# Kernel tuning notes

Measured on AMD Instinct MI355X. Metric: run time of the kernel, lower is better.

The kernel has to match this reference:

```python
import jax, jax.numpy as jnp
import numpy as np

N_NODES = 100000
BN_EPS = 1e-5


def gcn_conv(x, W, b, row, col, n_nodes):
    """GCNConv: D^{-1/2}(A+I)D^{-1/2} X W + b, edges row->col."""
    h = x @ W  # [N, out]
    # degree with self-loops, counted on destination side (symmetric for undirected)
    deg = jax.ops.segment_sum(jnp.ones(row.shape[0], dtype=x.dtype), col,
                              num_segments=n_nodes) + 1.0
    dis = jax.lax.rsqrt(deg)  # deg^{-1/2}
    coef = dis[row] * dis[col]  # [E]
    msg = h[row] * coef[:, None]  # gather + scale, [E, out]
    agg = jax.ops.segment_sum(msg, col, num_segments=n_nodes)
    # self-loop contribution: norm = dis[i]*dis[i]
    out = agg + h * (dis * dis)[:, None] + b
    return out


def batchnorm_train(x, gamma, beta):
    mean = jnp.mean(x, axis=0)
    var = jnp.mean(jnp.square(x - mean), axis=0)  # biased, training mode
    return (x - mean) * jax.lax.rsqrt(var + BN_EPS) * gamma + beta


def setup_inputs() -> dict:
    key = jax.random.key(0)
    ks = jax.random.split(key, 8)
    latent_dim, hidden_dim, input_dim = 64, 128, 128
    n_edges = 1600000
    x = jax.random.normal(ks[0], (N_NODES, latent_dim), dtype=jnp.float32)
    edge_index = jax.random.randint(ks[1], (2, n_edges), 0, N_NODES, dtype=jnp.int64)
    s1 = 1.0 / np.sqrt(latent_dim)
    s2 = 1.0 / np.sqrt(hidden_dim)
    W1 = jax.random.uniform(ks[2], (latent_dim, hidden_dim), jnp.float32, -s1, s1)
    b1 = jax.random.uniform(ks[3], (hidden_dim,), jnp.float32, -s1, s1)
    gamma = jnp.ones((hidden_dim,), jnp.float32)
    beta = jnp.zeros((hidden_dim,), jnp.float32)
    W2 = jax.random.uniform(ks[4], (hidden_dim, input_dim), jnp.float32, -s2, s2)
    b2 = jax.random.uniform(ks[5], (input_dim,), jnp.float32, -s2, s2)
    return {"quantized_f_embedding": x, "edge_index": edge_index,
            "W1": W1, "b1": b1, "gamma": gamma, "beta": beta,
            "W2": W2, "b2": b2}


def reference(quantized_f_embedding, edge_index, W1, b1, gamma, beta, W2, b2):
    row, col = edge_index[0], edge_index[1]
    h = gcn_conv(quantized_f_embedding, W1, b1, row, col, N_NODES)
    h = batchnorm_train(h, gamma, beta)
    out = gcn_conv(h, W2, b2, row, col, N_NODES)
    return out
```

## Files before the change

### kernel.cpp

```cpp
#include <hip/hip_runtime.h>

#define NN 100000
#define BN_EPS 1e-5f
#define NBK 782
#define CAP 2560
#define TILE 4096

#define NREP 16
#define CVT_BLKS 6250
#define AGG_BLKS 6250
#define ZERO_BLKS 80
#define PACK1_BLKS 32

typedef __attribute__((ext_vector_type(4))) _Float16 half4;
typedef __attribute__((ext_vector_type(8))) _Float16 half8;
typedef __attribute__((ext_vector_type(4))) float f32x4;


__global__ __launch_bounds__(256) void k_prep0(int* __restrict__ bcur,
                                               float* __restrict__ stats,
                                               const float* __restrict__ W1,
                                               _Float16* __restrict__ wp1) {
    const int b = blockIdx.x;
    const int t = threadIdx.x;
    if (b < ZERO_BLKS) {
        int i = b * 256 + t;
        if (i < 16384) bcur[i] = 0;
        else stats[i - 16384] = 0.f;
    } else {
        int i = (b - ZERO_BLKS) * 256 + t;
        int j = i & 7, l = (i >> 3) & 63, nt = (i >> 9) & 7, kt = i >> 12;
        int k = kt * 32 + ((l >> 4) << 3) + j;
        int n = nt * 16 + (l & 15);
        wp1[i] = (_Float16)W1[k * 128 + n];
    }
}


__global__ __launch_bounds__(256) void k_binc(const int* __restrict__ row,
                                              const int* __restrict__ col,
                                              int* __restrict__ bcur,
                                              int* __restrict__ ebuf,
                                              int E, int binBlks,
                                              const float* __restrict__ x,
                                              _Float16* __restrict__ xh) {
    __shared__ int hist[1024];
    __shared__ int excl[1024];
    __shared__ int cur[1024];
    __shared__ int gbase[1024];
    __shared__ int sc[256];
    __shared__ int staged[TILE];
    __shared__ unsigned short bkt[TILE];
    const int t = threadIdx.x;

    if (blockIdx.x >= binBlks) {
        int i = (blockIdx.x - binBlks) * 256 + t;
        float4 v = reinterpret_cast<const float4*>(x)[i];
        half4 o;
        o.x = (_Float16)v.x; o.y = (_Float16)v.y;
        o.z = (_Float16)v.z; o.w = (_Float16)v.w;
        reinterpret_cast<half4*>(xh)[i] = o;
        return;
    }

    const int base = blockIdx.x * TILE;
    const int nE = min(TILE, E - base);

    #pragma unroll
    for (int q = 0; q < 4; ++q) { hist[q * 256 + t] = 0; cur[q * 256 + t] = 0; }
    __syncthreads();

    int er[16], ec[16];
    #pragma unroll
    for (int k = 0; k < 16; ++k) {
        int idx = base + k * 256 + t;
        if (idx < E) {
            er[k] = row[idx];
            ec[k] = col[idx];
            atomicAdd(&hist[ec[k] >> 7], 1);
        } else {
            ec[k] = -1;
        }
    }
    __syncthreads();

    int h0 = hist[4 * t], h1 = hist[4 * t + 1], h2 = hist[4 * t + 2], h3 = hist[4 * t + 3];
    int p = h0 + h1 + h2 + h3;
    sc[t] = p;
    __syncthreads();
    for (int off = 1; off < 256; off <<= 1) {
        int add = (t >= off) ? sc[t - off] : 0;
        __syncthreads();
        sc[t] += add;
        __syncthreads();
    }
    int e0 = sc[t] - p;
    excl[4 * t]     = e0;
    excl[4 * t + 1] = e0 + h0;
    excl[4 * t + 2] = e0 + h0 + h1;
    excl[4 * t + 3] = e0 + h0 + h1 + h2;
    __syncthreads();

    for (int b = t; b < NBK; b += 256) {
        int h = hist[b];
        gbase[b] = h ? atomicAdd(&bcur[b * 16], h) : 0;
    }

    #pragma unroll
    for (int k = 0; k < 16; ++k) {
        int c = ec[k];
        if (c < 0) continue;
        int b = c >> 7;
        int slot = excl[b] + atomicAdd(&cur[b], 1);
        staged[slot] = (er[k] << 7) | (c & 127);
        bkt[slot] = (unsigned short)b;
    }
    __syncthreads();

    for (int i = t; i < nE; i += 256) {
        int b = bkt[i];
        int off = gbase[b] + (i - excl[b]);
        if (off < CAP) ebuf[b * CAP + off] = staged[i];
    }
}


__global__ __launch_bounds__(256) void k_csr(const int* __restrict__ bcur,
                                             const int* __restrict__ ebuf,
                                             int* __restrict__ rows,
                                             int* __restrict__ start,
                                             int* __restrict__ cnt,
                                             float* __restrict__ dis) {
    __shared__ int hist[128];
    __shared__ int lstart[128];
    __shared__ int cur[128];
    __shared__ int sc[256];
    const int b = blockIdx.x;
    const int t = threadIdx.x;
    const int fill = min(bcur[b * 16], CAP);

    if (t < 128) { hist[t] = 0; cur[t] = 0; }
    __syncthreads();

    int er[CAP / 256];
    #pragma unroll
    for (int k = 0; k < CAP / 256; ++k) {
        int i = k * 256 + t;
        if (i < fill) {
            er[k] = ebuf[b * CAP + i];
            atomicAdd(&hist[er[k] & 127], 1);
        }
    }
    __syncthreads();

    int v = (t < 128) ? hist[t] : 0;
    sc[t] = v;
    __syncthreads();
    for (int off = 1; off < 256; off <<= 1) {
        int add = (t >= off) ? sc[t - off] : 0;
        __syncthreads();
        sc[t] += add;
        __syncthreads();
    }
    if (t < 128) {
        lstart[t] = sc[t] - v;
        const int node = b * 128 + t;
        if (node < NN) {
            start[node] = b * CAP + (sc[t] - v);
            cnt[node] = v;
            dis[node] = rsqrtf((float)(v + 1));
        }
    }
    __syncthreads();

    #pragma unroll
    for (int k = 0; k < CAP / 256; ++k) {
        int i = k * 256 + t;
        if (i < fill) {
            int lc = er[k] & 127;
            int lpos = atomicAdd(&cur[lc], 1);
            rows[b * CAP + lstart[lc] + lpos] = er[k] >> 7;
        }
    }
}


__device__ __forceinline__ void fma_h4(float4& a, half4 v, float c) {
    a.x = fmaf((float)v.x, c, a.x);
    a.y = fmaf((float)v.y, c, a.y);
    a.z = fmaf((float)v.z, c, a.z);
    a.w = fmaf((float)v.w, c, a.w);
}

template<bool SUMC>
__device__ __forceinline__ void agg_body(int blk,
                                         const _Float16* __restrict__ xh,
                                         const int* __restrict__ rows,
                                         const int* __restrict__ start,
                                         const int* __restrict__ cnt,
                                         const float* __restrict__ dis,
                                         _Float16* __restrict__ agg,
                                         float* __restrict__ sumcoef) {
    constexpr int L = 16;
    const int t = threadIdx.x;
    const int g = t / L;
    const int fid = t % L;
    const int n = blk * 16 + g;
    if (n >= NN) return;
    const int s = start[n];
    const int c = cnt[n];
    const float dn = dis[n];
    const half4* X4 = reinterpret_cast<const half4*>(xh);
    half4 hv = X4[n * L + fid];
    const float dn2 = dn * dn;
    float4 acc = make_float4(dn2 * (float)hv.x, dn2 * (float)hv.y,
                             dn2 * (float)hv.z, dn2 * (float)hv.w);
    float sd = 0.f;
    const int* rp = rows + s;
    int k = 0;
    for (; k + 4 <= c; k += 4) {
        int r0 = rp[k], r1 = rp[k + 1], r2 = rp[k + 2], r3 = rp[k + 3];
        float d0 = dis[r0], d1 = dis[r1], d2 = dis[r2], d3 = dis[r3];
        half4 v0 = X4[r0 * L + fid];
        half4 v1 = X4[r1 * L + fid];
        half4 v2 = X4[r2 * L + fid];
        half4 v3 = X4[r3 * L + fid];
        fma_h4(acc, v0, d0 * dn);
        fma_h4(acc, v1, d1 * dn);
        fma_h4(acc, v2, d2 * dn);
        fma_h4(acc, v3, d3 * dn);
        sd += (d0 + d1) + (d2 + d3);
    }
    for (; k < c; ++k) {
        int r = rp[k];
        float dr = dis[r];
        half4 v = X4[r * L + fid];
        fma_h4(acc, v, dr * dn);
        sd += dr;
    }
    half4 o;
    o.x = (_Float16)acc.x; o.y = (_Float16)acc.y;
    o.z = (_Float16)acc.z; o.w = (_Float16)acc.w;
    reinterpret_cast<half4*>(agg)[n * L + fid] = o;
    if (SUMC && fid == 0) sumcoef[n] = dn * sd + dn2;
}


__device__ __forceinline__ void l2prep_body(int bb,
                                            const float* __restrict__ stats,
                                            const float* __restrict__ gamma,
                                            const float* __restrict__ beta,
                                            const float* __restrict__ b1,
                                            const float* __restrict__ W1,
                                            const float* __restrict__ W2,
                                            _Float16* __restrict__ wp12,
                                            float* __restrict__ sv) {
    __shared__ float s_[128];
    __shared__ float f2_[128];
    const int t = threadIdx.x;
    if (t < 128) {
        float sum = 0.f, sum2 = 0.f;
        #pragma unroll
        for (int r = 0; r < NREP; ++r) {
            sum  += stats[r * 256 + t];
            sum2 += stats[r * 256 + 128 + t];
        }
        const float n = (float)NN;
        float mean = sum / n;
        float var = sum2 / n - mean * mean;
        float sc = gamma[t] * rsqrtf(var + BN_EPS);
        s_[t] = sc;
        f2_[t] = b1[t] * sc + (beta[t] - mean * sc);
    }
    __syncthreads();
    if (bb < 32) {
        int i = bb * 256 + t;
        int j = i & 7, l = (i >> 3) & 63, nt = (i >> 9) & 7, kt = i >> 12;
        int kk = kt * 32 + ((l >> 4) << 3) + j;
        int nn = nt * 16 + (l & 15);
        float acc = 0.f;
        #pragma unroll 8
        for (int m = 0; m < 128; ++m)
            acc = fmaf(W1[kk * 128 + m] * s_[m], W2[m * 128 + nn], acc);
        wp12[i] = (_Float16)acc;
    } else if (t < 128) {
        float acc = 0.f;
        for (int k = 0; k < 128; ++k) acc = fmaf(f2_[k], W2[k * 128 + t], acc);
        sv[t] = acc;
    }
}


__global__ __launch_bounds__(256) void k_aggy(const _Float16* __restrict__ xh,
                                              const int* __restrict__ rows,
                                              const int* __restrict__ start,
                                              const int* __restrict__ cnt,
                                              const float* __restrict__ dis,
                                              _Float16* __restrict__ agg,
                                              float* __restrict__ sumcoef) {
    agg_body<true>(blockIdx.x, xh, rows, start, cnt, dis, agg, sumcoef);
}


__global__ __launch_bounds__(256) void k_aggz(const _Float16* __restrict__ y,
                                              const int* __restrict__ rows,
                                              const int* __restrict__ start,
                                              const int* __restrict__ cnt,
                                              const float* __restrict__ dis,
                                              _Float16* __restrict__ z,
                                              const float* __restrict__ stats,
                                              const float* __restrict__ gamma,
                                              const float* __restrict__ beta,
                                              const float* __restrict__ b1,
                                              const float* __restrict__ W1,
                                              const float* __restrict__ W2,
                                              _Float16* __restrict__ wp12,
                                              float* __restrict__ sv) {
    if (blockIdx.x < AGG_BLKS) {
        agg_body<false>(blockIdx.x, y, rows, start, cnt, dis, z, nullptr);
    } else {
        l2prep_body(blockIdx.x - AGG_BLKS, stats, gamma, beta, b1, W1, W2,
                    wp12, sv);
    }
}


template<bool FINAL>
__global__ __launch_bounds__(256) void k_mgemm(const _Float16* __restrict__ A,
                                               const _Float16* __restrict__ Wp,
                                               const float* __restrict__ bias,
                                               const float* __restrict__ sv,
                                               const float* __restrict__ sumcoef,
                                               float* __restrict__ out32,
                                               float* __restrict__ stats) {
    const int t = threadIdx.x;
    const int wv = t >> 6;
    const int ln = t & 63;
    const int cgrp = ln >> 4;
    const int ncol = ln & 15;
    const int r0 = blockIdx.x * 64 + wv * 16;
    const int arow = min(r0 + ncol, NN - 1);

    f32x4 acc[8];
    #pragma unroll
    for (int nt = 0; nt < 8; ++nt) acc[nt] = {0.f, 0.f, 0.f, 0.f};

    const half8* Ap = reinterpret_cast<const half8*>(A + arow * 64 + cgrp * 8);
    const half8* Bp = reinterpret_cast<const half8*>(Wp);

    #pragma unroll
    for (int kt = 0; kt < 2; ++kt) {
        half8 a = Ap[kt * 4];
        #pragma unroll
        for (int nt = 0; nt < 8; ++nt) {
            half8 b = Bp[(kt * 8 + nt) * 64 + ln];
            acc[nt] = __builtin_amdgcn_mfma_f32_16x16x32_f16(a, b, acc[nt], 0, 0, 0);
        }
    }

    if constexpr (!FINAL) {
        __shared__ float ls[4][128];
        __shared__ float ls2[4][128];
        #pragma unroll
        for (int nt = 0; nt < 8; ++nt) {
            const int n = nt * 16 + ncol;
            const float bn = bias[n];
            float s = 0.f, s2 = 0.f;
            #pragma unroll
            for (int j = 0; j < 4; ++j) {
                int gr = r0 + cgrp * 4 + j;
                float v = acc[nt][j] + bn;
                if (gr < NN) {
                    s += v;
                    s2 += v * v;
                }
            }
            s  += __shfl_xor(s, 16);  s  += __shfl_xor(s, 32);
            s2 += __shfl_xor(s2, 16); s2 += __shfl_xor(s2, 32);
            if (ln < 16) { ls[wv][n] = s; ls2[wv][n] = s2; }
        }
        __syncthreads();
        float* rep = stats + (blockIdx.x & (NREP - 1)) * 256;
        if (t < 128) {
            atomicAdd(&rep[t], ls[0][t] + ls[1][t] + ls[2][t] + ls[3][t]);
        } else {
            int u = t - 128;
            atomicAdd(&rep[128 + u], ls2[0][u] + ls2[1][u] + ls2[2][u] + ls2[3][u]);
        }
    } else {
        __shared__ float st[4][16][132];
        float scj[4];
        #pragma unroll
        for (int j = 0; j < 4; ++j) scj[j] = sumcoef[min(r0 + cgrp * 4 + j, NN - 1)];
        #pragma unroll
        for (int nt = 0; nt < 8; ++nt) {
            const int n = nt * 16 + ncol;
            const float svn = sv[n];
            const float bn = bias[n];
            #pragma unroll
            for (int j = 0; j < 4; ++j)
                st[wv][cgrp * 4 + j][n] = acc[nt][j] + scj[j] * svn + bn;
        }
        __syncthreads();
        #pragma unroll
        for (int i = 0; i < 8; ++i) {
            int idx = i * 64 + ln;
            int rr = idx >> 5;
            int c4 = idx & 31;
            int gr = r0 + rr;
            if (gr < NN) {
                float4 v = *reinterpret_cast<float4*>(&st[wv][rr][c4 * 4]);
                *reinterpret_cast<float4*>(&out32[gr * 128 + c4 * 4]) = v;
            }
        }
    }
}


extern "C" void kernel_launch(void* const* d_in, const int* in_sizes, int n_in,
                              void* d_out, int out_size, void* d_ws, size_t ws_size,
                              hipStream_t stream) {
    const float* x     = (const float*)d_in[0];
    const int*   ei    = (const int*)d_in[1];
    const float* W1    = (const float*)d_in[2];
    const float* b1    = (const float*)d_in[3];
    const float* gamma = (const float*)d_in[4];
    const float* beta  = (const float*)d_in[5];
    const float* W2    = (const float*)d_in[6];
    const float* b2    = (const float*)d_in[7];
    float* out = (float*)d_out;

    const int E = in_sizes[1] / 2;
    const int* row = ei;
    const int* col = ei + E;
    const int binBlks = (E + TILE - 1) / TILE;

    int*   bcur    = (int*)d_ws;
    int*   cnt     = bcur + 16384;
    int*   start   = cnt + 102400;
    float* dis     = (float*)(start + 102400);
    float* stats   = dis + 102400;
    float* sv      = stats + 4096;
    float* sumcoef = stats + 5120;
    _Float16* wp1  = (_Float16*)(sumcoef + 102400);
    _Float16* wp12 = wp1 + 8192;
    int*   rows    = (int*)(wp12 + 8192);
    int*   Rbase   = rows + NBK * CAP;
    _Float16* xh   = (_Float16*)Rbase;
    int*   ebuf    = Rbase + 3276800;
    _Float16* y    = (_Float16*)(ebuf + NBK * CAP);
    _Float16* z    = xh;

    k_prep0<<<ZERO_BLKS + PACK1_BLKS, 256, 0, stream>>>(bcur, stats, W1, wp1);
    k_binc<<<binBlks + CVT_BLKS, 256, 0, stream>>>(row, col, bcur, ebuf, E,
                                                   binBlks, x, xh);
    k_csr<<<NBK, 256, 0, stream>>>(bcur, ebuf, rows, start, cnt, dis);

    k_aggy<<<AGG_BLKS, 256, 0, stream>>>(xh, rows, start, cnt, dis, y, sumcoef);
    k_mgemm<false><<<(NN + 63) / 64, 256, 0, stream>>>(y, wp1, b1, nullptr,
                                                       nullptr, nullptr, stats);

    k_aggz<<<AGG_BLKS + 33, 256, 0, stream>>>(y, rows, start, cnt, dis, z,
                                              stats, gamma, beta, b1, W1, W2,
                                              wp12, sv);

    k_mgemm<true><<<(NN + 63) / 64, 256, 0, stream>>>(z, wp12, b2, sv,
                                                      sumcoef, out, nullptr);
}
```

Measured before the change: 147.6 us.

## Fuse neighbor aggregation into MFMA GEMM kernels via shared-memory tile

```diff
diff --git a/kernel.cpp b/kernel.cpp
--- a/kernel.cpp
+++ b/kernel.cpp
@@ -8,33 +8,12 @@
 
 #define NREP 16
 #define CVT_BLKS 6250
-#define AGG_BLKS 6250
-#define ZERO_BLKS 80
 #define PACK1_BLKS 32
+#define GEMM_BLKS 1563
 
 typedef __attribute__((ext_vector_type(4))) _Float16 half4;
 typedef __attribute__((ext_vector_type(8))) _Float16 half8;
 typedef __attribute__((ext_vector_type(4))) float f32x4;
-
-
-__global__ __launch_bounds__(256) void k_prep0(int* __restrict__ bcur,
-                                               float* __restrict__ stats,
-                                               const float* __restrict__ W1,
-                                               _Float16* __restrict__ wp1) {
-    const int b = blockIdx.x;
-    const int t = threadIdx.x;
-    if (b < ZERO_BLKS) {
-        int i = b * 256 + t;
-        if (i < 16384) bcur[i] = 0;
-        else stats[i - 16384] = 0.f;
-    } else {
-        int i = (b - ZERO_BLKS) * 256 + t;
-        int j = i & 7, l = (i >> 3) & 63, nt = (i >> 9) & 7, kt = i >> 12;
-        int k = kt * 32 + ((l >> 4) << 3) + j;
-        int n = nt * 16 + (l & 15);
-        wp1[i] = (_Float16)W1[k * 128 + n];
-    }
-}
 
 
 __global__ __launch_bounds__(256) void k_binc(const int* __restrict__ row,
@@ -43,7 +22,9 @@
                                               int* __restrict__ ebuf,
                                               int E, int binBlks,
                                               const float* __restrict__ x,
-                                              _Float16* __restrict__ xh) {
+                                              _Float16* __restrict__ xh,
+                                              const float* __restrict__ W1,
+                                              _Float16* __restrict__ wp1) {
     __shared__ int hist[1024];
     __shared__ int excl[1024];
     __shared__ int cur[1024];
@@ -54,12 +35,21 @@
     const int t = threadIdx.x;
 
     if (blockIdx.x >= binBlks) {
-        int i = (blockIdx.x - binBlks) * 256 + t;
-        float4 v = reinterpret_cast<const float4*>(x)[i];
-        half4 o;
-        o.x = (_Float16)v.x; o.y = (_Float16)v.y;
-        o.z = (_Float16)v.z; o.w = (_Float16)v.w;
-        reinterpret_cast<half4*>(xh)[i] = o;
+        int rb = blockIdx.x - binBlks;
+        if (rb < CVT_BLKS) {
+            int i = rb * 256 + t;
+            float4 v = reinterpret_cast<const float4*>(x)[i];
+            half4 o;
+            o.x = (_Float16)v.x; o.y = (_Float16)v.y;
+            o.z = (_Float16)v.z; o.w = (_Float16)v.w;
+            reinterpret_cast<half4*>(xh)[i] = o;
+        } else {
+            int i = (rb - CVT_BLKS) * 256 + t;
+            int j = i & 7, l = (i >> 3) & 63, nt = (i >> 9) & 7, kt = i >> 12;
+            int k = kt * 32 + ((l >> 4) << 3) + j;
+            int n = nt * 16 + (l & 15);
+            wp1[i] = (_Float16)W1[k * 128 + n];
+        }
         return;
     }
 
@@ -185,78 +175,17 @@
 }
 
 
-__device__ __forceinline__ void fma_h4(float4& a, half4 v, float c) {
-    a.x = fmaf((float)v.x, c, a.x);
-    a.y = fmaf((float)v.y, c, a.y);
-    a.z = fmaf((float)v.z, c, a.z);
-    a.w = fmaf((float)v.w, c, a.w);
-}
-
-template<bool SUMC>
-__device__ __forceinline__ void agg_body(int blk,
-                                         const _Float16* __restrict__ xh,
-                                         const int* __restrict__ rows,
-                                         const int* __restrict__ start,
-                                         const int* __restrict__ cnt,
-                                         const float* __restrict__ dis,
-                                         _Float16* __restrict__ agg,
-                                         float* __restrict__ sumcoef) {
-    constexpr int L = 16;
-    const int t = threadIdx.x;
-    const int g = t / L;
-    const int fid = t % L;
-    const int n = blk * 16 + g;
-    if (n >= NN) return;
-    const int s = start[n];
-    const int c = cnt[n];
-    const float dn = dis[n];
-    const half4* X4 = reinterpret_cast<const half4*>(xh);
-    half4 hv = X4[n * L + fid];
-    const float dn2 = dn * dn;
-    float4 acc = make_float4(dn2 * (float)hv.x, dn2 * (float)hv.y,
-                             dn2 * (float)hv.z, dn2 * (float)hv.w);
-    float sd = 0.f;
-    const int* rp = rows + s;
-    int k = 0;
-    for (; k + 4 <= c; k += 4) {
-        int r0 = rp[k], r1 = rp[k + 1], r2 = rp[k + 2], r3 = rp[k + 3];
-        float d0 = dis[r0], d1 = dis[r1], d2 = dis[r2], d3 = dis[r3];
-        half4 v0 = X4[r0 * L + fid];
-        half4 v1 = X4[r1 * L + fid];
-        half4 v2 = X4[r2 * L + fid];
-        half4 v3 = X4[r3 * L + fid];
-        fma_h4(acc, v0, d0 * dn);
-        fma_h4(acc, v1, d1 * dn);
-        fma_h4(acc, v2, d2 * dn);
-        fma_h4(acc, v3, d3 * dn);
-        sd += (d0 + d1) + (d2 + d3);
-    }
-    for (; k < c; ++k) {
-        int r = rp[k];
-        float dr = dis[r];
-        half4 v = X4[r * L + fid];
-        fma_h4(acc, v, dr * dn);
-        sd += dr;
-    }
-    half4 o;
-    o.x = (_Float16)acc.x; o.y = (_Float16)acc.y;
-    o.z = (_Float16)acc.z; o.w = (_Float16)acc.w;
-    reinterpret_cast<half4*>(agg)[n * L + fid] = o;
-    if (SUMC && fid == 0) sumcoef[n] = dn * sd + dn2;
-}
-
-
-__device__ __forceinline__ void l2prep_body(int bb,
-                                            const float* __restrict__ stats,
-                                            const float* __restrict__ gamma,
-                                            const float* __restrict__ beta,
-                                            const float* __restrict__ b1,
-                                            const float* __restrict__ W1,
-                                            const float* __restrict__ W2,
-                                            _Float16* __restrict__ wp12,
-                                            float* __restrict__ sv) {
+__global__ __launch_bounds__(256) void k_l2prep(const float* __restrict__ stats,
+                                                const float* __restrict__ gamma,
+                                                const float* __restrict__ beta,
+                                                const float* __restrict__ b1,
+                                                const float* __restrict__ W1,
+                                                const float* __restrict__ W2,
+                                                _Float16* __restrict__ wp12,
+                                                float* __restrict__ sv) {
     __shared__ float s_[128];
     __shared__ float f2_[128];
+    const int bb = blockIdx.x;
     const int t = threadIdx.x;
     if (t < 128) {
         float sum = 0.f, sum2 = 0.f;
@@ -291,66 +220,101 @@
 }
 
 
-__global__ __launch_bounds__(256) void k_aggy(const _Float16* __restrict__ xh,
-                                              const int* __restrict__ rows,
-                                              const int* __restrict__ start,
-                                              const int* __restrict__ cnt,
-                                              const float* __restrict__ dis,
-                                              _Float16* __restrict__ agg,
-                                              float* __restrict__ sumcoef) {
-    agg_body<true>(blockIdx.x, xh, rows, start, cnt, dis, agg, sumcoef);
-}
-
-
-__global__ __launch_bounds__(256) void k_aggz(const _Float16* __restrict__ y,
-                                              const int* __restrict__ rows,
-                                              const int* __restrict__ start,
-                                              const int* __restrict__ cnt,
-                                              const float* __restrict__ dis,
-                                              _Float16* __restrict__ z,
-                                              const float* __restrict__ stats,
-                                              const float* __restrict__ gamma,
-                                              const float* __restrict__ beta,
-                                              const float* __restrict__ b1,
-                                              const float* __restrict__ W1,
-                                              const float* __restrict__ W2,
-                                              _Float16* __restrict__ wp12,
-                                              float* __restrict__ sv) {
-    if (blockIdx.x < AGG_BLKS) {
-        agg_body<false>(blockIdx.x, y, rows, start, cnt, dis, z, nullptr);
-    } else {
-        l2prep_body(blockIdx.x - AGG_BLKS, stats, gamma, beta, b1, W1, W2,
-                    wp12, sv);
-    }
-}
-
+__device__ __forceinline__ void fma_h4(float4& a, half4 v, float c) {
+    a.x = fmaf((float)v.x, c, a.x);
+    a.y = fmaf((float)v.y, c, a.y);
+    a.z = fmaf((float)v.z, c, a.z);
+    a.w = fmaf((float)v.w, c, a.w);
+}
 
 template<bool FINAL>
-__global__ __launch_bounds__(256) void k_mgemm(const _Float16* __restrict__ A,
+__global__ __launch_bounds__(256) void k_agemm(const _Float16* __restrict__ X,
+                                               const int* __restrict__ rows,
+                                               const int* __restrict__ start,
+                                               const int* __restrict__ cnt,
+                                               const float* __restrict__ dis,
                                                const _Float16* __restrict__ Wp,
                                                const float* __restrict__ bias,
                                                const float* __restrict__ sv,
-                                               const float* __restrict__ sumcoef,
+                                               const float* __restrict__ sumcoef_in,
+                                               _Float16* __restrict__ yout,
+                                               float* __restrict__ sumcoef_out,
                                                float* __restrict__ out32,
                                                float* __restrict__ stats) {
+    __shared__ __align__(16) _Float16 tile[64][72];
     const int t = threadIdx.x;
+    const int r0 = blockIdx.x * 64;
+
+    {
+        const int g = t >> 4;
+        const int fid = t & 15;
+        const half4* X4 = reinterpret_cast<const half4*>(X);
+        #pragma unroll
+        for (int q = 0; q < 4; ++q) {
+            const int n = r0 + q * 16 + g;
+            const int lr = q * 16 + g;
+            if (n < NN) {
+                const int s = start[n];
+                const int c = cnt[n];
+                const float dn = dis[n];
+                half4 hv = X4[n * 16 + fid];
+                const float dn2 = dn * dn;
+                float4 acc = make_float4(dn2 * (float)hv.x, dn2 * (float)hv.y,
+                                         dn2 * (float)hv.z, dn2 * (float)hv.w);
+                float sd = 0.f;
+                const int* rp = rows + s;
+                int k = 0;
+                for (; k + 4 <= c; k += 4) {
+                    int rr0 = rp[k], rr1 = rp[k + 1], rr2 = rp[k + 2], rr3 = rp[k + 3];
+                    float d0 = dis[rr0], d1 = dis[rr1], d2 = dis[rr2], d3 = dis[rr3];
+                    half4 v0 = X4[rr0 * 16 + fid];
+                    half4 v1 = X4[rr1 * 16 + fid];
+                    half4 v2 = X4[rr2 * 16 + fid];
+                    half4 v3 = X4[rr3 * 16 + fid];
+                    fma_h4(acc, v0, d0 * dn);
+                    fma_h4(acc, v1, d1 * dn);
+                    fma_h4(acc, v2, d2 * dn);
+                    fma_h4(acc, v3, d3 * dn);
+                    sd += (d0 + d1) + (d2 + d3);
+                }
+                for (; k < c; ++k) {
+                    int r = rp[k];
+                    float dr = dis[r];
+                    half4 v = X4[r * 16 + fid];
+                    fma_h4(acc, v, dr * dn);
+                    sd += dr;
+                }
+                half4 o;
+                o.x = (_Float16)acc.x; o.y = (_Float16)acc.y;
+                o.z = (_Float16)acc.z; o.w = (_Float16)acc.w;
+                *reinterpret_cast<half4*>(&tile[lr][fid * 4]) = o;
+                if constexpr (!FINAL) {
+                    reinterpret_cast<half4*>(yout)[n * 16 + fid] = o;
+                    if (fid == 0) sumcoef_out[n] = dn * sd + dn2;
+                }
+            } else {
+                half4 zz = {(_Float16)0.f, (_Float16)0.f, (_Float16)0.f, (_Float16)0.f};
+                *reinterpret_cast<half4*>(&tile[lr][fid * 4]) = zz;
+            }
+        }
+    }
+    __syncthreads();
+
     const int wv = t >> 6;
     const int ln = t & 63;
     const int cgrp = ln >> 4;
     const int ncol = ln & 15;
-    const int r0 = blockIdx.x * 64 + wv * 16;
-    const int arow = min(r0 + ncol, NN - 1);
+    const int row0 = r0 + wv * 16;
 
     f32x4 acc[8];
     #pragma unroll
     for (int nt = 0; nt < 8; ++nt) acc[nt] = {0.f, 0.f, 0.f, 0.f};
 
-    const half8* Ap = reinterpret_cast<const half8*>(A + arow * 64 + cgrp * 8);
     const half8* Bp = reinterpret_cast<const half8*>(Wp);
 
     #pragma unroll
     for (int kt = 0; kt < 2; ++kt) {
-        half8 a = Ap[kt * 4];
+        half8 a = *reinterpret_cast<const half8*>(&tile[wv * 16 + ncol][kt * 32 + cgrp * 8]);
         #pragma unroll
         for (int nt = 0; nt < 8; ++nt) {
             half8 b = Bp[(kt * 8 + nt) * 64 + ln];
@@ -368,7 +332,7 @@
             float s = 0.f, s2 = 0.f;
             #pragma unroll
             for (int j = 0; j < 4; ++j) {
-                int gr = r0 + cgrp * 4 + j;
+                int gr = row0 + cgrp * 4 + j;
                 float v = acc[nt][j] + bn;
                 if (gr < NN) {
                     s += v;
@@ -388,29 +352,18 @@
             atomicAdd(&rep[128 + u], ls2[0][u] + ls2[1][u] + ls2[2][u] + ls2[3][u]);
         }
     } else {
-        __shared__ float st[4][16][132];
         float scj[4];
         #pragma unroll
-        for (int j = 0; j < 4; ++j) scj[j] = sumcoef[min(r0 + cgrp * 4 + j, NN - 1)];
+        for (int j = 0; j < 4; ++j) scj[j] = sumcoef_in[min(row0 + cgrp * 4 + j, NN - 1)];
         #pragma unroll
         for (int nt = 0; nt < 8; ++nt) {
             const int n = nt * 16 + ncol;
             const float svn = sv[n];
             const float bn = bias[n];
             #pragma unroll
-            for (int j = 0; j < 4; ++j)
-                st[wv][cgrp * 4 + j][n] = acc[nt][j] + scj[j] * svn + bn;
-        }
-        __syncthreads();
-        #pragma unroll
-        for (int i = 0; i < 8; ++i) {
-            int idx = i * 64 + ln;
-            int rr = idx >> 5;
-            int c4 = idx & 31;
-            int gr = r0 + rr;
-            if (gr < NN) {
-                float4 v = *reinterpret_cast<float4*>(&st[wv][rr][c4 * 4]);
-                *reinterpret_cast<float4*>(&out32[gr * 128 + c4 * 4]) = v;
+            for (int j = 0; j < 4; ++j) {
+                int gr = row0 + cgrp * 4 + j;
+                if (gr < NN) out32[gr * 128 + n] = acc[nt][j] + scj[j] * svn + bn;
             }
         }
     }
@@ -436,12 +389,12 @@
     const int binBlks = (E + TILE - 1) / TILE;
 
     int*   bcur    = (int*)d_ws;
-    int*   cnt     = bcur + 16384;
+    float* stats   = (float*)(bcur + 16384);
+    int*   cnt     = (int*)(stats + 4096);
     int*   start   = cnt + 102400;
     float* dis     = (float*)(start + 102400);
-    float* stats   = dis + 102400;
-    float* sv      = stats + 4096;
-    float* sumcoef = stats + 5120;
+    float* sv      = dis + 102400;
+    float* sumcoef = sv + 1024;
     _Float16* wp1  = (_Float16*)(sumcoef + 102400);
     _Float16* wp12 = wp1 + 8192;
     int*   rows    = (int*)(wp12 + 8192);
@@ -449,21 +402,19 @@
     _Float16* xh   = (_Float16*)Rbase;
     int*   ebuf    = Rbase + 3276800;
     _Float16* y    = (_Float16*)(ebuf + NBK * CAP);
-    _Float16* z    = xh;
-
-    k_prep0<<<ZERO_BLKS + PACK1_BLKS, 256, 0, stream>>>(bcur, stats, W1, wp1);
-    k_binc<<<binBlks + CVT_BLKS, 256, 0, stream>>>(row, col, bcur, ebuf, E,
-                                                   binBlks, x, xh);
+
+    hipMemsetAsync(bcur, 0, 20480 * sizeof(int), stream);
+    k_binc<<<binBlks + CVT_BLKS + PACK1_BLKS, 256, 0, stream>>>(
+        row, col, bcur, ebuf, E, binBlks, x, xh, W1, wp1);
     k_csr<<<NBK, 256, 0, stream>>>(bcur, ebuf, rows, start, cnt, dis);
 
-    k_aggy<<<AGG_BLKS, 256, 0, stream>>>(xh, rows, start, cnt, dis, y, sumcoef);
-    k_mgemm<false><<<(NN + 63) / 64, 256, 0, stream>>>(y, wp1, b1, nullptr,
-                                                       nullptr, nullptr, stats);
-
-    k_aggz<<<AGG_BLKS + 33, 256, 0, stream>>>(y, rows, start, cnt, dis, z,
-                                              stats, gamma, beta, b1, W1, W2,
-                                              wp12, sv);
-
-    k_mgemm<true><<<(NN + 63) / 64, 256, 0, stream>>>(z, wp12, b2, sv,
-                                                      sumcoef, out, nullptr);
-}
+    k_agemm<false><<<GEMM_BLKS, 256, 0, stream>>>(xh, rows, start, cnt, dis,
+                                                  wp1, b1, nullptr, nullptr,
+                                                  y, sumcoef, nullptr, stats);
+
+    k_l2prep<<<33, 256, 0, stream>>>(stats, gamma, beta, b1, W1, W2, wp12, sv);
+
+    k_agemm<true><<<GEMM_BLKS, 256, 0, stream>>>(y, rows, start, cnt, dis,
+                                                 wp12, b2, sv, sumcoef,
+                                                 nullptr, nullptr, out, nullptr);
+}
```

Measured after the change: 190.4 us. +29.0%, slower.

## Fuse BN-stats GEMM with second aggregation using a device-wide completion counter

Applied to the files above, without the earlier changes.

```diff
diff --git a/kernel.cpp b/kernel.cpp
--- a/kernel.cpp
+++ b/kernel.cpp
@@ -9,32 +9,15 @@
 #define NREP 16
 #define CVT_BLKS 6250
 #define AGG_BLKS 6250
-#define ZERO_BLKS 80
 #define PACK1_BLKS 32
+#define STATS_BLKS 1563
+
+#define COMBO_L2_OFF (STATS_BLKS + AGG_BLKS)
+#define COMBO_BLKS (COMBO_L2_OFF + 33)
 
 typedef __attribute__((ext_vector_type(4))) _Float16 half4;
 typedef __attribute__((ext_vector_type(8))) _Float16 half8;
 typedef __attribute__((ext_vector_type(4))) float f32x4;
-
-
-__global__ __launch_bounds__(256) void k_prep0(int* __restrict__ bcur,
-                                               float* __restrict__ stats,
-                                               const float* __restrict__ W1,
-                                               _Float16* __restrict__ wp1) {
-    const int b = blockIdx.x;
-    const int t = threadIdx.x;
-    if (b < ZERO_BLKS) {
-        int i = b * 256 + t;
-        if (i < 16384) bcur[i] = 0;
-        else stats[i - 16384] = 0.f;
-    } else {
-        int i = (b - ZERO_BLKS) * 256 + t;
-        int j = i & 7, l = (i >> 3) & 63, nt = (i >> 9) & 7, kt = i >> 12;
-        int k = kt * 32 + ((l >> 4) << 3) + j;
-        int n = nt * 16 + (l & 15);
-        wp1[i] = (_Float16)W1[k * 128 + n];
-    }
-}
 
 
 __global__ __launch_bounds__(256) void k_binc(const int* __restrict__ row,
@@ -43,7 +26,9 @@
                                               int* __restrict__ ebuf,
                                               int E, int binBlks,
                                               const float* __restrict__ x,
-                                              _Float16* __restrict__ xh) {
+                                              _Float16* __restrict__ xh,
+                                              const float* __restrict__ W1,
+                                              _Float16* __restrict__ wp1) {
     __shared__ int hist[1024];
     __shared__ int excl[1024];
     __shared__ int cur[1024];
@@ -54,12 +39,21 @@
     const int t = threadIdx.x;
 
     if (blockIdx.x >= binBlks) {
-        int i = (blockIdx.x - binBlks) * 256 + t;
-        float4 v = reinterpret_cast<const float4*>(x)[i];
-        half4 o;
-        o.x = (_Float16)v.x; o.y = (_Float16)v.y;
-        o.z = (_Float16)v.z; o.w = (_Float16)v.w;
-        reinterpret_cast<half4*>(xh)[i] = o;
+        int rb = blockIdx.x - binBlks;
+        if (rb < CVT_BLKS) {
+            int i = rb * 256 + t;
+            float4 v = reinterpret_cast<const float4*>(x)[i];
+            half4 o;
+            o.x = (_Float16)v.x; o.y = (_Float16)v.y;
+            o.z = (_Float16)v.z; o.w = (_Float16)v.w;
+            reinterpret_cast<half4*>(xh)[i] = o;
+        } else {
+            int i = (rb - CVT_BLKS) * 256 + t;
+            int j = i & 7, l = (i >> 3) & 63, nt = (i >> 9) & 7, kt = i >> 12;
+            int k = kt * 32 + ((l >> 4) << 3) + j;
+            int n = nt * 16 + (l & 15);
+            wp1[i] = (_Float16)W1[k * 128 + n];
+        }
         return;
     }
 
@@ -246,51 +240,6 @@
 }
 
 
-__device__ __forceinline__ void l2prep_body(int bb,
-                                            const float* __restrict__ stats,
-                                            const float* __restrict__ gamma,
-                                            const float* __restrict__ beta,
-                                            const float* __restrict__ b1,
-                                            const float* __restrict__ W1,
-                                            const float* __restrict__ W2,
-                                            _Float16* __restrict__ wp12,
-                                            float* __restrict__ sv) {
-    __shared__ float s_[128];
-    __shared__ float f2_[128];
-    const int t = threadIdx.x;
-    if (t < 128) {
-        float sum = 0.f, sum2 = 0.f;
-        #pragma unroll
-        for (int r = 0; r < NREP; ++r) {
-            sum  += stats[r * 256 + t];
-            sum2 += stats[r * 256 + 128 + t];
-        }
-        const float n = (float)NN;
-        float mean = sum / n;
-        float var = sum2 / n - mean * mean;
-        float sc = gamma[t] * rsqrtf(var + BN_EPS);
-        s_[t] = sc;
-        f2_[t] = b1[t] * sc + (beta[t] - mean * sc);
-    }
-    __syncthreads();
-    if (bb < 32) {
-        int i = bb * 256 + t;
-        int j = i & 7, l = (i >> 3) & 63, nt = (i >> 9) & 7, kt = i >> 12;
-        int kk = kt * 32 + ((l >> 4) << 3) + j;
-        int nn = nt * 16 + (l & 15);
-        float acc = 0.f;
-        #pragma unroll 8
-        for (int m = 0; m < 128; ++m)
-            acc = fmaf(W1[kk * 128 + m] * s_[m], W2[m * 128 + nn], acc);
-        wp12[i] = (_Float16)acc;
-    } else if (t < 128) {
-        float acc = 0.f;
-        for (int k = 0; k < 128; ++k) acc = fmaf(f2_[k], W2[k * 128 + t], acc);
-        sv[t] = acc;
-    }
-}
-
-
 __global__ __launch_bounds__(256) void k_aggy(const _Float16* __restrict__ xh,
                                               const int* __restrict__ rows,
                                               const int* __restrict__ start,
@@ -302,69 +251,56 @@
 }
 
 
-__global__ __launch_bounds__(256) void k_aggz(const _Float16* __restrict__ y,
-                                              const int* __restrict__ rows,
-                                              const int* __restrict__ start,
-                                              const int* __restrict__ cnt,
-                                              const float* __restrict__ dis,
-                                              _Float16* __restrict__ z,
-                                              const float* __restrict__ stats,
-                                              const float* __restrict__ gamma,
-                                              const float* __restrict__ beta,
-                                              const float* __restrict__ b1,
-                                              const float* __restrict__ W1,
-                                              const float* __restrict__ W2,
-                                              _Float16* __restrict__ wp12,
-                                              float* __restrict__ sv) {
-    if (blockIdx.x < AGG_BLKS) {
-        agg_body<false>(blockIdx.x, y, rows, start, cnt, dis, z, nullptr);
-    } else {
-        l2prep_body(blockIdx.x - AGG_BLKS, stats, gamma, beta, b1, W1, W2,
-                    wp12, sv);
-    }
-}
-
-
-template<bool FINAL>
-__global__ __launch_bounds__(256) void k_mgemm(const _Float16* __restrict__ A,
-                                               const _Float16* __restrict__ Wp,
-                                               const float* __restrict__ bias,
-                                               const float* __restrict__ sv,
-                                               const float* __restrict__ sumcoef,
-                                               float* __restrict__ out32,
-                                               float* __restrict__ stats) {
+__global__ __launch_bounds__(256) void k_combo(const _Float16* __restrict__ y,
+                                               const int* __restrict__ rows,
+                                               const int* __restrict__ start,
+                                               const int* __restrict__ cnt,
+                                               const float* __restrict__ dis,
+                                               _Float16* __restrict__ z,
+                                               const _Float16* __restrict__ wp1,
+                                               const float* __restrict__ b1,
+                                               float* __restrict__ stats,
+                                               int* __restrict__ done,
+                                               const float* __restrict__ gamma,
+                                               const float* __restrict__ beta,
+                                               const float* __restrict__ W1,
+                                               const float* __restrict__ W2,
+                                               _Float16* __restrict__ wp12,
+                                               float* __restrict__ sv) {
+    const int bid = blockIdx.x;
     const int t = threadIdx.x;
-    const int wv = t >> 6;
-    const int ln = t & 63;
-    const int cgrp = ln >> 4;
-    const int ncol = ln & 15;
-    const int r0 = blockIdx.x * 64 + wv * 16;
-    const int arow = min(r0 + ncol, NN - 1);
-
-    f32x4 acc[8];
-    #pragma unroll
-    for (int nt = 0; nt < 8; ++nt) acc[nt] = {0.f, 0.f, 0.f, 0.f};
-
-    const half8* Ap = reinterpret_cast<const half8*>(A + arow * 64 + cgrp * 8);
-    const half8* Bp = reinterpret_cast<const half8*>(Wp);
-
-    #pragma unroll
-    for (int kt = 0; kt < 2; ++kt) {
-        half8 a = Ap[kt * 4];
+
+    if (bid < STATS_BLKS) {
+        const int wv = t >> 6;
+        const int ln = t & 63;
+        const int cgrp = ln >> 4;
+        const int ncol = ln & 15;
+        const int r0 = bid * 64 + wv * 16;
+        const int arow = min(r0 + ncol, NN - 1);
+
+        f32x4 acc[8];
         #pragma unroll
-        for (int nt = 0; nt < 8; ++nt) {
-            half8 b = Bp[(kt * 8 + nt) * 64 + ln];
-            acc[nt] = __builtin_amdgcn_mfma_f32_16x16x32_f16(a, b, acc[nt], 0, 0, 0);
-        }
-    }
-
-    if constexpr (!FINAL) {
+        for (int nt = 0; nt < 8; ++nt) acc[nt] = {0.f, 0.f, 0.f, 0.f};
+
+        const half8* Ap = reinterpret_cast<const half8*>(y + arow * 64 + cgrp * 8);
+        const half8* Bp = reinterpret_cast<const half8*>(wp1);
+
+        #pragma unroll
+        for (int kt = 0; kt < 2; ++kt) {
+            half8 a = Ap[kt * 4];
+            #pragma unroll
+            for (int nt = 0; nt < 8; ++nt) {
+                half8 b = Bp[(kt * 8 + nt) * 64 + ln];
+                acc[nt] = __builtin_amdgcn_mfma_f32_16x16x32_f16(a, b, acc[nt], 0, 0, 0);
+            }
+        }
+
         __shared__ float ls[4][128];
         __shared__ float ls2[4][128];
         #pragma unroll
         for (int nt = 0; nt < 8; ++nt) {
             const int n = nt * 16 + ncol;
-            const float bn = bias[n];
+            const float bn = b1[n];
             float s = 0.f, s2 = 0.f;
             #pragma unroll
             for (int j = 0; j < 4; ++j) {
@@ -380,38 +316,119 @@
             if (ln < 16) { ls[wv][n] = s; ls2[wv][n] = s2; }
         }
         __syncthreads();
-        float* rep = stats + (blockIdx.x & (NREP - 1)) * 256;
+        float* rep = stats + (bid & (NREP - 1)) * 256;
         if (t < 128) {
             atomicAdd(&rep[t], ls[0][t] + ls[1][t] + ls[2][t] + ls[3][t]);
         } else {
             int u = t - 128;
             atomicAdd(&rep[128 + u], ls2[0][u] + ls2[1][u] + ls2[2][u] + ls2[3][u]);
         }
+        __syncthreads();
+        __threadfence();
+        if (t == 0) atomicAdd(done, 1);
+    } else if (bid < COMBO_L2_OFF) {
+        agg_body<false>(bid - STATS_BLKS, y, rows, start, cnt, dis, z, nullptr);
     } else {
-        __shared__ float st[4][16][132];
-        float scj[4];
-        #pragma unroll
-        for (int j = 0; j < 4; ++j) scj[j] = sumcoef[min(r0 + cgrp * 4 + j, NN - 1)];
+        const int bb = bid - COMBO_L2_OFF;
+        if (t == 0) {
+            while (__hip_atomic_load(done, __ATOMIC_ACQUIRE,
+                                     __HIP_MEMORY_SCOPE_AGENT) < STATS_BLKS)
+                __builtin_amdgcn_s_sleep(10);
+        }
+        __syncthreads();
+
+        __shared__ float s_[128];
+        __shared__ float f2_[128];
+        if (t < 128) {
+            float sum = 0.f, sum2 = 0.f;
+            #pragma unroll
+            for (int r = 0; r < NREP; ++r) {
+                sum  += __hip_atomic_load(&stats[r * 256 + t], __ATOMIC_RELAXED,
+                                          __HIP_MEMORY_SCOPE_AGENT);
+                sum2 += __hip_atomic_load(&stats[r * 256 + 128 + t], __ATOMIC_RELAXED,
+                                          __HIP_MEMORY_SCOPE_AGENT);
+            }
+            const float n = (float)NN;
+            float mean = sum / n;
+            float var = sum2 / n - mean * mean;
+            float sc = gamma[t] * rsqrtf(var + BN_EPS);
+            s_[t] = sc;
+            f2_[t] = b1[t] * sc + (beta[t] - mean * sc);
+        }
+        __syncthreads();
+        if (bb < 32) {
+            int i = bb * 256 + t;
+            int j = i & 7, l = (i >> 3) & 63, nt = (i >> 9) & 7, kt = i >> 12;
+            int kk = kt * 32 + ((l >> 4) << 3) + j;
+            int nn = nt * 16 + (l & 15);
+            float acc = 0.f;
+            #pragma unroll 8
+            for (int m = 0; m < 128; ++m)
+                acc = fmaf(W1[kk * 128 + m] * s_[m], W2[m * 128 + nn], acc);
+            wp12[i] = (_Float16)acc;
+        } else if (t < 128) {
+            float acc = 0.f;
+            for (int k = 0; k < 128; ++k) acc = fmaf(f2_[k], W2[k * 128 + t], acc);
+            sv[t] = acc;
+        }
+    }
+}
+
+
+__global__ __launch_bounds__(256) void k_mgemmf(const _Float16* __restrict__ A,
+                                                const _Float16* __restrict__ Wp,
+                                                const float* __restrict__ bias,
+                                                const float* __restrict__ sv,
+                                                const float* __restrict__ sumcoef,
+                                                float* __restrict__ out32) {
+    const int t = threadIdx.x;
+    const int wv = t >> 6;
+    const int ln = t & 63;
+    const int cgrp = ln >> 4;
+    const int ncol = ln & 15;
+    const int r0 = blockIdx.x * 64 + wv * 16;
+    const int arow = min(r0 + ncol, NN - 1);
+
+    f32x4 acc[8];
+    #pragma unroll
+    for (int nt = 0; nt < 8; ++nt) acc[nt] = {0.f, 0.f, 0.f, 0.f};
+
+    const half8* Ap = reinterpret_cast<const half8*>(A + arow * 64 + cgrp * 8);
+    const half8* Bp = reinterpret_cast<const half8*>(Wp);
+
+    #pragma unroll
+    for (int kt = 0; kt < 2; ++kt) {
+        half8 a = Ap[kt * 4];
         #pragma unroll
         for (int nt = 0; nt < 8; ++nt) {
-            const int n = nt * 16 + ncol;
-            const float svn = sv[n];
-            const float bn = bias[n];
-            #pragma unroll
-            for (int j = 0; j < 4; ++j)
-                st[wv][cgrp * 4 + j][n] = acc[nt][j] + scj[j] * svn + bn;
-        }
-        __syncthreads();
+            half8 b = Bp[(kt * 8 + nt) * 64 + ln];
+            acc[nt] = __builtin_amdgcn_mfma_f32_16x16x32_f16(a, b, acc[nt], 0, 0, 0);
+        }
+    }
+
+    __shared__ float st[4][16][132];
+    float scj[4];
+    #pragma unroll
+    for (int j = 0; j < 4; ++j) scj[j] = sumcoef[min(r0 + cgrp * 4 + j, NN - 1)];
+    #pragma unroll
+    for (int nt = 0; nt < 8; ++nt) {
+        const int n = nt * 16 + ncol;
+        const float svn = sv[n];
+        const float bn = bias[n];
         #pragma unroll
-        for (int i = 0; i < 8; ++i) {
-            int idx = i * 64 + ln;
-            int rr = idx >> 5;
-            int c4 = idx & 31;
-            int gr = r0 + rr;
-            if (gr < NN) {
-                float4 v = *reinterpret_cast<float4*>(&st[wv][rr][c4 * 4]);
-                *reinterpret_cast<float4*>(&out32[gr * 128 + c4 * 4]) = v;
-            }
+        for (int j = 0; j < 4; ++j)
+            st[wv][cgrp * 4 + j][n] = acc[nt][j] + scj[j] * svn + bn;
+    }
+    __syncthreads();
+    #pragma unroll
+    for (int i = 0; i < 8; ++i) {
+        int idx = i * 64 + ln;
+        int rr = idx >> 5;
+        int c4 = idx & 31;
+        int gr = r0 + rr;
+        if (gr < NN) {
+            float4 v = *reinterpret_cast<float4*>(&st[wv][rr][c4 * 4]);
+            *reinterpret_cast<float4*>(&out32[gr * 128 + c4 * 4]) = v;
         }
     }
 }
@@ -436,12 +453,13 @@
     const int binBlks = (E + TILE - 1) / TILE;
 
     int*   bcur    = (int*)d_ws;
-    int*   cnt     = bcur + 16384;
+    float* stats   = (float*)(bcur + 16384);
+    int*   done    = (int*)(stats + 4096);
+    int*   cnt     = done + 16;
     int*   start   = cnt + 102400;
     float* dis     = (float*)(start + 102400);
-    float* stats   = dis + 102400;
-    float* sv      = stats + 4096;
-    float* sumcoef = stats + 5120;
+    float* sv      = dis + 102400;
+    float* sumcoef = sv + 1024;
     _Float16* wp1  = (_Float16*)(sumcoef + 102400);
     _Float16* wp12 = wp1 + 8192;
     int*   rows    = (int*)(wp12 + 8192);
@@ -451,19 +469,16 @@
     _Float16* y    = (_Float16*)(ebuf + NBK * CAP);
     _Float16* z    = xh;
 
-    k_prep0<<<ZERO_BLKS + PACK1_BLKS, 256, 0, stream>>>(bcur, stats, W1, wp1);
-    k_binc<<<binBlks + CVT_BLKS, 256, 0, stream>>>(row, col, bcur, ebuf, E,
-                                                   binBlks, x, xh);
+    hipMemsetAsync(bcur, 0, (16384 + 4096 + 16) * sizeof(int), stream);
+    k_binc<<<binBlks + CVT_BLKS + PACK1_BLKS, 256, 0, stream>>>(
+        row, col, bcur, ebuf, E, binBlks, x, xh, W1, wp1);
     k_csr<<<NBK, 256, 0, stream>>>(bcur, ebuf, rows, start, cnt, dis);
 
     k_aggy<<<AGG_BLKS, 256, 0, stream>>>(xh, rows, start, cnt, dis, y, sumcoef);
-    k_mgemm<false><<<(NN + 63) / 64, 256, 0, stream>>>(y, wp1, b1, nullptr,
-                                                       nullptr, nullptr, stats);
-
-    k_aggz<<<AGG_BLKS + 33, 256, 0, stream>>>(y, rows, start, cnt, dis, z,
-                                              stats, gamma, beta, b1, W1, W2,
-                                              wp12, sv);
-
-    k_mgemm<true><<<(NN + 63) / 64, 256, 0, stream>>>(z, wp12, b2, sv,
-                                                      sumcoef, out, nullptr);
-}
+
+    k_combo<<<COMBO_BLKS, 256, 0, stream>>>(y, rows, start, cnt, dis, z,
+                                            wp1, b1, stats, done,
+                                            gamma, beta, W1, W2, wp12, sv);
+
+    k_mgemmf<<<STATS_BLKS, 256, 0, stream>>>(z, wp12, b2, sv, sumcoef, out);
+}
```

Result: slower. 294.5 us (+99.5%).
